# Kernel tuning notes

Hardware: AMD Instinct MI355X
Metric: run time of the kernel (lower is better)

## Reference

```python
import jax, jax.numpy as jnp
import numpy as np

POOL = 14
STRIDES = (4, 8, 16, 32)


def _roi_align(feat, boxes, bidx, scale, out=POOL):
    """Bilinear RoIAlign (1 sample per bin center). feat: [N,C,H,W], boxes: [M,4] image coords."""
    N, C, H, W = feat.shape
    b = boxes * scale
    x1, y1, x2, y2 = b[:, 0], b[:, 1], b[:, 2], b[:, 3]
    g = (jnp.arange(out, dtype=feat.dtype) + 0.5) / out
    xs = x1[:, None] + g[None, :] * (x2 - x1)[:, None]  # [M,out]
    ys = y1[:, None] + g[None, :] * (y2 - y1)[:, None]  # [M,out]
    x0f = jnp.floor(xs); y0f = jnp.floor(ys)
    lx = xs - x0f; ly = ys - y0f
    x0 = jnp.clip(x0f, 0, W - 1).astype(jnp.int32)
    x1i = jnp.clip(x0f + 1, 0, W - 1).astype(jnp.int32)
    y0 = jnp.clip(y0f, 0, H - 1).astype(jnp.int32)
    y1i = jnp.clip(y0f + 1, 0, H - 1).astype(jnp.int32)
    ft = jnp.transpose(feat, (0, 2, 3, 1))  # NHWC for trailing-channel gather
    bi = bidx[:, None, None]

    def gat(yy, xx):
        return ft[bi, yy[:, :, None], xx[:, None, :]]  # [M,out,out,C]

    wly = ly[:, :, None, None]; wlx = lx[:, None, :, None]
    val = (gat(y0, x0) * (1 - wly) * (1 - wlx)
           + gat(y0, x1i) * (1 - wly) * wlx
           + gat(y1i, x0) * wly * (1 - wlx)
           + gat(y1i, x1i) * wly * wlx)
    return jnp.transpose(val, (0, 3, 1, 2))  # [M,C,out,out]


def _fpn_levels(boxes, img_h, img_w):
    """Per-box FPN level: floor(4 + log2(sqrt(wh)/alpha)) mapped to pyramid index [0,3]."""
    alpha = 224.0 / 800.0 * float(min(img_h, img_w))
    bw = jnp.abs(boxes[:, 2] - boxes[:, 0])
    bh = jnp.abs(boxes[:, 3] - boxes[:, 1])
    s = jnp.sqrt(jnp.maximum(bw * bh, 1e-6))
    k = jnp.floor(4.0 + jnp.log2(s / alpha))
    return jnp.clip(k - 2.0, 0, 3).astype(jnp.int32)


def setup_inputs() -> dict:
    key = jax.random.key(0)
    ks = jax.random.split(key, 16)
    N, C, M, NCLS, HID = 2, 512, 512, 81, 1024
    p2 = jax.random.normal(ks[0], (N, C, 200, 200), jnp.float32)
    p3 = jax.random.normal(ks[1], (N, C, 100, 100), jnp.float32)
    p4 = jax.random.normal(ks[2], (N, C, 50, 50), jnp.float32)
    p5 = jax.random.normal(ks[3], (N, C, 25, 25), jnp.float32)
    cx = jax.random.uniform(ks[4], (M,), minval=100.0, maxval=700.0)
    cy = jax.random.uniform(ks[5], (M,), minval=100.0, maxval=700.0)
    bw = jax.random.uniform(ks[6], (M,), minval=32.0, maxval=400.0)
    bh = jax.random.uniform(ks[7], (M,), minval=32.0, maxval=400.0)
    boxes = jnp.stack([jnp.clip(cx - bw / 2, 0, 800), jnp.clip(cy - bh / 2, 0, 800),
                       jnp.clip(cx + bw / 2, 0, 800), jnp.clip(cy + bh / 2, 0, 800)], axis=1)
    batch_idx = jnp.repeat(jnp.arange(N, dtype=jnp.int32), M // N)
    w_fc1 = jax.random.normal(ks[8], (C * POOL * POOL, HID), jnp.float32) * 0.01
    b_fc1 = jnp.zeros((HID,), jnp.float32)
    w_cls = jax.random.normal(ks[9], (HID, NCLS), jnp.float32) * 0.05
    b_cls = jnp.zeros((NCLS,), jnp.float32)
    w_box = jax.random.normal(ks[10], (HID, NCLS), jnp.float32) * 0.05
    b_box = jnp.zeros((NCLS,), jnp.float32)
    w_conv = jax.random.normal(ks[11], (256, C, 3, 3), jnp.float32) * 0.02
    b_conv = jnp.zeros((256,), jnp.float32)
    w_mfc = jax.random.normal(ks[12], (256, NCLS), jnp.float32) * 0.05
    b_mfc = jnp.zeros((NCLS,), jnp.float32)
    return dict(p2=p2, p3=p3, p4=p4, p5=p5, boxes=boxes, batch_idx=batch_idx,
                w_fc1=w_fc1, b_fc1=b_fc1, w_cls=w_cls, b_cls=b_cls,
                w_box=w_box, b_box=b_box, w_conv=w_conv, b_conv=b_conv,
                w_mfc=w_mfc, b_mfc=b_mfc, img_h=800, img_w=800)


def reference(p2, p3, p4, p5, boxes, batch_idx, w_fc1, b_fc1, w_cls, b_cls,
              w_box, b_box, w_conv, b_conv, w_mfc, b_mfc, img_h, img_w):
    N = p2.shape[0]
    C = p2.shape[1]
    M = boxes.shape[0]
    num_classes = w_cls.shape[1]
    lvl = _fpn_levels(boxes, img_h, img_w)
    pooled = jnp.zeros((M, C, POOL, POOL), p2.dtype)
    for l, (feat, stride) in enumerate(zip([p2, p3, p4, p5], STRIDES)):
        pl = _roi_align(feat, boxes, batch_idx, 1.0 / stride)
        pooled = jnp.where((lvl == l)[:, None, None, None], pl, pooled)
    # cls / bbox head
    flat = pooled.reshape(M, -1)
    h = jax.nn.relu(flat @ w_fc1 + b_fc1)
    prob_cls = jax.nn.softmax(h @ w_cls + b_cls, axis=-1)
    reg_bbox = h @ w_box + b_box
    # mask head
    z = jax.lax.conv_general_dilated(pooled, w_conv, (1, 1), 'SAME',
                                     dimension_numbers=('NCHW', 'OIHW', 'NCHW'))
    z = jax.nn.relu(z + b_conv[None, :, None, None])
    prob_mask = jax.nn.sigmoid(jnp.mean(z, axis=(2, 3)) @ w_mfc + b_mfc)
    return (prob_cls.reshape(N, -1, num_classes),
            reg_bbox.reshape(N, -1, num_classes),
            prob_mask.reshape(N, -1, num_classes))
```

## Files before the change

kernel.cpp:

```cpp
#include <hip/hip_runtime.h>
#include <hip/hip_bf16.h>

#define POOLN 14
#define NBINS 196
#define CCH 512
#define MROIS 512
#define HIDD 1024
#define NCLS 81
#define KTOT 100352

typedef short short8 __attribute__((ext_vector_type(8)));
typedef __bf16 bf16x8 __attribute__((ext_vector_type(8)));
typedef float float4v __attribute__((ext_vector_type(4)));

__device__ __forceinline__ float4v mfma_bf16(bf16x8 a, bf16x8 b, float4v c) {
    return __builtin_amdgcn_mfma_f32_16x16x32_bf16(a, b, c, 0, 0, 0);
}

__device__ __forceinline__ unsigned short f2bf(float v) {
    __hip_bfloat16 h = __float2bfloat16(v);
    return __builtin_bit_cast(unsigned short, h);
}
__device__ __forceinline__ float bflo(unsigned int u) {
    return __builtin_bit_cast(float, u << 16);
}
__device__ __forceinline__ float bfhi(unsigned int u) {
    return __builtin_bit_cast(float, u & 0xFFFF0000u);
}

__device__ __forceinline__ void gload16(const void* g, void* l) {
    __builtin_amdgcn_global_load_lds(
        (const __attribute__((address_space(1))) unsigned int*)g,
        (__attribute__((address_space(3))) unsigned int*)l, 16, 0, 0);
}

__global__ void k_tr(const float* __restrict__ p2, const float* __restrict__ p3,
                     const float* __restrict__ p4, const float* __restrict__ p5,
                     unsigned short* __restrict__ f0, unsigned short* __restrict__ f1,
                     unsigned short* __restrict__ f2, unsigned short* __restrict__ f3) {
    __shared__ float tile[64 * 65];
    int pt = blockIdx.x;
    int n  = blockIdx.y >> 3;
    int c0 = (blockIdx.y & 7) * 64;
    const float* src; unsigned short* dst; int P;
    if (pt < 625)      { src = p2; dst = f0; P = 40000; }
    else if (pt < 782) { src = p3; dst = f1; P = 10000; pt -= 625; }
    else if (pt < 822) { src = p4; dst = f2; P = 2500;  pt -= 782; }
    else               { src = p5; dst = f3; P = 625;   pt -= 822; }
    int p0 = pt * 64;
    int t = threadIdx.x;
    #pragma unroll
    for (int i = 0; i < 16; ++i) {
        int idx = i * 256 + t;
        int pl = idx & 63, cl = idx >> 6;
        int p = p0 + pl;
        float v = 0.f;
        if (p < P) v = src[(size_t)(n * 512 + c0 + cl) * (size_t)P + p];
        tile[cl * 65 + pl] = v;
    }
    __syncthreads();
    #pragma unroll
    for (int i = 0; i < 8; ++i) {
        int idx = i * 256 + t;
        int cp = idx & 31, pl = idx >> 5;
        int p = p0 + pl;
        if (p < P) {
            unsigned int lo = (unsigned int)f2bf(tile[(cp * 2) * 65 + pl]);
            unsigned int hi = (unsigned int)f2bf(tile[(cp * 2 + 1) * 65 + pl]);
            *(unsigned int*)(dst + ((size_t)(n * (size_t)P + p) * 512 + c0 + cp * 2)) = lo | (hi << 16);
        }
    }
}

__global__ void k_roi(const unsigned short* __restrict__ f0, const unsigned short* __restrict__ f1,
                      const unsigned short* __restrict__ f2, const unsigned short* __restrict__ f3,
                      const float* __restrict__ boxes, const int* __restrict__ bidx,
                      const int* __restrict__ imh, const int* __restrict__ imw,
                      unsigned short* __restrict__ pooled) {
    int m = blockIdx.x;
    int t = threadIdx.x;
    float b0 = boxes[m*4+0], b1 = boxes[m*4+1], b2 = boxes[m*4+2], b3 = boxes[m*4+3];
    int ih = imh[0], iw = imw[0];
    float alpha = (224.0f/800.0f) * (float)(ih < iw ? ih : iw);
    float bw = fabsf(b2-b0), bh = fabsf(b3-b1);
    float s = sqrtf(fmaxf(bw*bh, 1e-6f));
    float kf = floorf(4.0f + log2f(s/alpha)) - 2.0f;
    int lvl = (int)fminf(fmaxf(kf, 0.0f), 3.0f);
    const unsigned short* f = lvl==0 ? f0 : (lvl==1 ? f1 : (lvl==2 ? f2 : f3));
    int W = 200 >> lvl;
    int P = W * W;
    float scale = 1.0f / (float)(4 << lvl);
    float x1s=b0*scale, y1s=b1*scale, x2s=b2*scale, y2s=b3*scale;
    const unsigned short* fb = f + (size_t)bidx[m] * (size_t)P * 512 + 2*t;
    unsigned short* outp = pooled + (size_t)m * NBINS * CCH + 2*t;
    float Wm1 = (float)(W-1);
    for (int py = 0; py < POOLN; ++py) {
        float gy = ((float)py + 0.5f) / 14.0f;
        float ys = y1s + gy * (y2s - y1s);
        float y0f = floorf(ys);
        float ly = ys - y0f;
        int y0 = (int)fminf(fmaxf(y0f, 0.0f), Wm1);
        int y1 = (int)fminf(fmaxf(y0f+1.0f, 0.0f), Wm1);
        #pragma unroll
        for (int px = 0; px < POOLN; ++px) {
            float gx = ((float)px + 0.5f) / 14.0f;
            float xs = x1s + gx * (x2s - x1s);
            float x0f = floorf(xs);
            float lx = xs - x0f;
            int x0 = (int)fminf(fmaxf(x0f, 0.0f), Wm1);
            int x1 = (int)fminf(fmaxf(x0f+1.0f, 0.0f), Wm1);
            unsigned int u00 = *(const unsigned int*)(fb + (size_t)(y0*W + x0) * 512);
            unsigned int u01 = *(const unsigned int*)(fb + (size_t)(y0*W + x1) * 512);
            unsigned int u10 = *(const unsigned int*)(fb + (size_t)(y1*W + x0) * 512);
            unsigned int u11 = *(const unsigned int*)(fb + (size_t)(y1*W + x1) * 512);
            float w00 = (1.0f-ly)*(1.0f-lx), w01 = (1.0f-ly)*lx;
            float w10 = ly*(1.0f-lx),        w11 = ly*lx;
            float vlo = bflo(u00)*w00 + bflo(u01)*w01 + bflo(u10)*w10 + bflo(u11)*w11;
            float vhi = bfhi(u00)*w00 + bfhi(u01)*w01 + bfhi(u10)*w10 + bfhi(u11)*w11;
            unsigned int r = (unsigned int)f2bf(vlo) | ((unsigned int)f2bf(vhi) << 16);
            *(unsigned int*)(outp + (size_t)(py*POOLN + px) * CCH) = r;
        }
    }
}

__global__ void k_pack_wfc1(const float* __restrict__ w, unsigned short* __restrict__ pk) {
    int g = blockIdx.x * 256 + threadIdx.x;
    int n = g & 1023;
    int k8 = g >> 10;
    int kp = k8 << 3;
    int p  = kp >> 9;
    int cc = kp & 511;
    short8 hv;
    #pragma unroll
    for (int j = 0; j < 8; ++j) {
        float v = w[(size_t)((cc+j)*NBINS + p) * HIDD + n];
        hv[j] = (short)f2bf(v);
    }
    *(short8*)(pk + (size_t)g * 8) = hv;
}

__global__ void k_pack_wconv(const float* __restrict__ w, unsigned short* __restrict__ wb) {
    int g = blockIdx.x * 256 + threadIdx.x;
    int c  = g & 511;
    int oc = (g >> 9) & 255;
    int kk = g >> 17;
    wb[g] = f2bf(w[(size_t)(oc*512 + c)*9 + kk]);
}

__launch_bounds__(256, 1)
__global__ void k_fc1(const unsigned short* __restrict__ A, const unsigned short* __restrict__ B,
                      float* __restrict__ part) {
    __shared__ unsigned short As[256*32];
    __shared__ unsigned short Bs[128*32];
    int t = threadIdx.x;
    int n0 = blockIdx.x * 128;
    int m0 = blockIdx.y * 256;
    int kz = blockIdx.z;
    int wave = t >> 6, ln = t & 63, ln15 = ln & 15, q = ln >> 4;
    int wr = (wave >> 1) * 128, wc = (wave & 1) * 64;
    int seg = ln & 3, rsub = ln >> 2;
    float4v acc[8][4];
    #pragma unroll
    for (int i = 0; i < 8; ++i)
        #pragma unroll
        for (int j = 0; j < 4; ++j) acc[i][j] = (float4v){0.f,0.f,0.f,0.f};
    int kbase = kz * 6272;
    for (int it = 0; it < 196; ++it) {
        int k0 = kbase + it*32;
        __syncthreads();
        #pragma unroll
        for (int i = 0; i < 4; ++i) {
            int row = i*64 + wave*16 + rsub;
            gload16(A + (size_t)(m0+row)*KTOT + k0 + seg*8, &As[(i*64 + wave*16)*32]);
        }
        #pragma unroll
        for (int i = 0; i < 2; ++i) {
            int nl = i*64 + wave*16 + rsub;
            gload16(B + ((size_t)((k0 >> 3) + seg)*1024 + n0 + nl)*8, &Bs[(i*64 + wave*16)*32]);
        }
        __syncthreads();
        bf16x8 bfr[4];
        #pragma unroll
        for (int ct = 0; ct < 4; ++ct)
            bfr[ct] = *(const bf16x8*)(&Bs[(wc + ct*16 + ln15)*32 + q*8]);
        #pragma unroll
        for (int rt = 0; rt < 8; ++rt) {
            bf16x8 af = *(const bf16x8*)(&As[(wr + rt*16 + ln15)*32 + q*8]);
            #pragma unroll
            for (int ct = 0; ct < 4; ++ct)
                acc[rt][ct] = mfma_bf16(af, bfr[ct], acc[rt][ct]);
        }
    }
    float* po = part + (size_t)kz * (MROIS*HIDD);
    #pragma unroll
    for (int rt = 0; rt < 8; ++rt)
        #pragma unroll
        for (int ct = 0; ct < 4; ++ct)
            #pragma unroll
            for (int r = 0; r < 4; ++r) {
                int row = m0 + wr + rt*16 + q*4 + r;
                int col = n0 + wc + ct*16 + ln15;
                po[(size_t)row*HIDD + col] = acc[rt][ct][r];
            }
}

__global__ void k_fc1_red(const float* __restrict__ part, const float* __restrict__ bias,
                          float* __restrict__ h) {
    int idx = blockIdx.x*256 + threadIdx.x;
    float s = 0.f;
    #pragma unroll
    for (int k = 0; k < 16; ++k) s += part[(size_t)k*524288 + idx];
    h[idx] = fmaxf(s + bias[idx & 1023], 0.f);
}

__launch_bounds__(512, 1)
__global__ void k_conv(const unsigned short* __restrict__ pooled, const unsigned short* __restrict__ wb,
                       const float* __restrict__ bconv, float* __restrict__ zmean) {
    __shared__ unsigned short As[208*32];
    __shared__ float sred[2][256];
    int m = blockIdx.x;
    int t = threadIdx.x;
    int wave = t >> 6, ln = t & 63, ln15 = ln & 15, q = ln >> 4;
    int og = wave & 3, mh = wave >> 2;
    int oc0 = og * 64;
    int rt0 = mh * 7;
    float4v acc[4][7];
    #pragma unroll
    for (int i = 0; i < 4; ++i)
        #pragma unroll
        for (int j = 0; j < 7; ++j) acc[i][j] = (float4v){0.f,0.f,0.f,0.f};
    const unsigned short* pm = pooled + (size_t)m * NBINS * CCH;
    const short8 Z8 = {0,0,0,0,0,0,0,0};
    int seg = ln & 3, rsub = ln >> 2;
    for (int ch = 0; ch < 16; ++ch) {
        int c0 = ch * 32;
        __syncthreads();
        #pragma unroll
        for (int i = 0; i < 2; ++i) {
            int wg = i*8 + wave;
            if (wg < 13) {
                int row = wg*16 + rsub;
                int rrow = row < 196 ? row : 195;
                gload16(pm + (size_t)rrow*CCH + c0 + seg*8, &As[(wg*16)*32]);
            }
        }
        __syncthreads();
        #pragma unroll
        for (int pos = 0; pos < 9; ++pos) {
            int dy = pos/3 - 1, dx = pos%3 - 1;
            bf16x8 bfr[4];
            #pragma unroll
            for (int oct = 0; oct < 4; ++oct)
                bfr[oct] = *(const bf16x8*)(wb + (size_t)(pos*256 + oc0 + oct*16 + ln15)*CCH + c0 + q*8);
            #pragma unroll
            for (int rr = 0; rr < 7; ++rr) {
                int rt = rt0 + rr;
                int p = rt*16 + ln15;
                int y = p / 14, x = p % 14;
                int yy = y + dy, xx = x + dx;
                bool valid = (p < 196) && ((unsigned)yy < 14u) && ((unsigned)xx < 14u);
                bf16x8 af = __builtin_bit_cast(bf16x8, Z8);
                if (valid) af = *(const bf16x8*)(&As[(yy*14+xx)*32 + q*8]);
                #pragma unroll
                for (int oct = 0; oct < 4; ++oct)
                    acc[oct][rr] = mfma_bf16(af, bfr[oct], acc[oct][rr]);
            }
        }
    }
    #pragma unroll
    for (int oct = 0; oct < 4; ++oct) {
        float b = bconv[oc0 + oct*16 + ln15];
        float s = 0.f;
        #pragma unroll
        for (int rr = 0; rr < 7; ++rr) {
            int rt = rt0 + rr;
            #pragma unroll
            for (int r = 0; r < 4; ++r) {
                int p = rt*16 + q*4 + r;
                if (p < 196) s += fmaxf(acc[oct][rr][r] + b, 0.f);
            }
        }
        s += __shfl_xor(s, 16, 64);
        s += __shfl_xor(s, 32, 64);
        if (ln < 16) sred[mh][oc0 + oct*16 + ln15] = s;
    }
    __syncthreads();
    if (t < 256) zmean[m*256 + t] = (sred[0][t] + sred[1][t]) * (1.0f/196.0f);
}

__global__ void k_cls(const float* __restrict__ h, const float* __restrict__ wcls,
                      const float* __restrict__ bcls, const float* __restrict__ wbox,
                      const float* __restrict__ bbox, float* __restrict__ out) {
    __shared__ float hs[HIDD];
    __shared__ float sc[NCLS];
    __shared__ float red[2];
    int m = blockIdx.x, t = threadIdx.x;
    #pragma unroll
    for (int i = 0; i < 8; ++i) hs[t + i*128] = h[(size_t)m*HIDD + t + i*128];
    __syncthreads();
    if (t < NCLS) {
        float ac = bcls[t], ab = bbox[t];
        #pragma unroll 4
        for (int k = 0; k < HIDD; ++k) {
            float hv = hs[k];
            ac += hv * wcls[k*NCLS + t];
            ab += hv * wbox[k*NCLS + t];
        }
        sc[t] = ac;
        out[41472 + m*NCLS + t] = ab;
    }
    __syncthreads();
    if (t == 0) {
        float mx = -3.0e38f;
        for (int i = 0; i < NCLS; ++i) mx = fmaxf(mx, sc[i]);
        red[0] = mx;
    }
    __syncthreads();
    if (t < NCLS) sc[t] = expf(sc[t] - red[0]);
    __syncthreads();
    if (t == 0) {
        float sm = 0.f;
        for (int i = 0; i < NCLS; ++i) sm += sc[i];
        red[1] = sm;
    }
    __syncthreads();
    if (t < NCLS) out[m*NCLS + t] = sc[t] / red[1];
}

__global__ void k_mask(const float* __restrict__ zmean, const float* __restrict__ wm,
                       const float* __restrict__ bm, float* __restrict__ out) {
    __shared__ float zs[256];
    int m = blockIdx.x, t = threadIdx.x;
    #pragma unroll
    for (int i = 0; i < 2; ++i) zs[t + i*128] = zmean[m*256 + t + i*128];
    __syncthreads();
    if (t < NCLS) {
        float a = bm[t];
        #pragma unroll 4
        for (int k = 0; k < 256; ++k) a += zs[k] * wm[k*NCLS + t];
        out[82944 + m*NCLS + t] = 1.0f / (1.0f + expf(-a));
    }
}

extern "C" void kernel_launch(void* const* d_in, const int* in_sizes, int n_in,
                              void* d_out, int out_size, void* d_ws, size_t ws_size,
                              hipStream_t stream) {
    (void)in_sizes; (void)n_in; (void)out_size; (void)ws_size;
    const float* p2    = (const float*)d_in[0];
    const float* p3    = (const float*)d_in[1];
    const float* p4    = (const float*)d_in[2];
    const float* p5    = (const float*)d_in[3];
    const float* boxes = (const float*)d_in[4];
    const int*   bidx  = (const int*)d_in[5];
    const float* wfc1  = (const float*)d_in[6];
    const float* bfc1  = (const float*)d_in[7];
    const float* wcls  = (const float*)d_in[8];
    const float* bcls  = (const float*)d_in[9];
    const float* wbox  = (const float*)d_in[10];
    const float* bbox  = (const float*)d_in[11];
    const float* wconv = (const float*)d_in[12];
    const float* bconv = (const float*)d_in[13];
    const float* wmfc  = (const float*)d_in[14];
    const float* bmfc  = (const float*)d_in[15];
    const int*   imh   = (const int*)d_in[16];
    const int*   imw   = (const int*)d_in[17];

    char* ws = (char*)d_ws;
    unsigned short* fpt0     = (unsigned short*)(ws);
    unsigned short* fpt1     = (unsigned short*)(ws + 81920000ull);
    unsigned short* fpt2     = (unsigned short*)(ws + 102400000ull);
    unsigned short* fpt3     = (unsigned short*)(ws + 107520000ull);
    unsigned short* packedB  = (unsigned short*)(ws);
    float*          partials = (float*)(ws + 205520896ull);
    float*          hbuf     = (float*)(ws + 239075328ull);
    float*          zmean    = (float*)(ws + 241172480ull);
    unsigned short* wconvb   = (unsigned short*)(ws + 241696768ull);
    unsigned short* pooled   = (unsigned short*)(ws + 244056064ull);
    float*          out      = (float*)d_out;

    hipLaunchKernelGGL(k_tr, dim3(832, 16), dim3(256), 0, stream,
                       p2, p3, p4, p5, fpt0, fpt1, fpt2, fpt3);
    hipLaunchKernelGGL(k_roi, dim3(512), dim3(256), 0, stream,
                       fpt0, fpt1, fpt2, fpt3, boxes, bidx, imh, imw, pooled);
    hipLaunchKernelGGL(k_pack_wfc1,  dim3(50176), dim3(256), 0, stream, wfc1, packedB);
    hipLaunchKernelGGL(k_pack_wconv, dim3(4608),  dim3(256), 0, stream, wconv, wconvb);
    hipLaunchKernelGGL(k_conv, dim3(512),  dim3(512), 0, stream, pooled, wconvb, bconv, zmean);
    hipLaunchKernelGGL(k_fc1,  dim3(8, 2, 16), dim3(256), 0, stream, pooled, packedB, partials);
    hipLaunchKernelGGL(k_fc1_red, dim3(2048), dim3(256), 0, stream, partials, bfc1, hbuf);
    hipLaunchKernelGGL(k_cls,  dim3(512), dim3(128), 0, stream, hbuf, wcls, bcls, wbox, bbox, out);
    hipLaunchKernelGGL(k_mask, dim3(512), dim3(128), 0, stream, zmean, wmfc, bmfc, out);
}
```

Baseline: 1.600 ms.

## Use MFMA for cls/box head and split conv by halves with padded LDS

```diff
diff --git a/kernel.cpp b/kernel.cpp
--- a/kernel.cpp
+++ b/kernel.cpp
@@ -139,12 +139,28 @@
     *(short8*)(pk + (size_t)g * 8) = hv;
 }
 
-__global__ void k_pack_wconv(const float* __restrict__ w, unsigned short* __restrict__ wb) {
+__global__ void k_pack_wconv(const float* __restrict__ w, unsigned short* __restrict__ wb,
+                             float* __restrict__ zmean) {
+    if (blockIdx.x >= 4608) {
+        int z = (blockIdx.x - 4608) * 256 + threadIdx.x;
+        zmean[z] = 0.f;
+        return;
+    }
     int g = blockIdx.x * 256 + threadIdx.x;
     int c  = g & 511;
     int oc = (g >> 9) & 255;
     int kk = g >> 17;
     wb[g] = f2bf(w[(size_t)(oc*512 + c)*9 + kk]);
+}
+
+__global__ void k_pack_whead(const float* __restrict__ wcls, const float* __restrict__ wbox,
+                             unsigned short* __restrict__ whb) {
+    int g = blockIdx.x * 256 + threadIdx.x;
+    int n = g >> 10, k = g & 1023;
+    float v = 0.f;
+    if (n < 81)       v = wcls[k*NCLS + n];
+    else if (n < 162) v = wbox[k*NCLS + (n-81)];
+    whb[g] = f2bf(v);
 }
 
 __launch_bounds__(256, 1)
@@ -205,62 +221,70 @@
 }
 
 __global__ void k_fc1_red(const float* __restrict__ part, const float* __restrict__ bias,
-                          float* __restrict__ h) {
+                          unsigned short* __restrict__ hb) {
     int idx = blockIdx.x*256 + threadIdx.x;
     float s = 0.f;
     #pragma unroll
     for (int k = 0; k < 16; ++k) s += part[(size_t)k*524288 + idx];
-    h[idx] = fmaxf(s + bias[idx & 1023], 0.f);
-}
-
-__launch_bounds__(512, 1)
+    hb[idx] = f2bf(fmaxf(s + bias[idx & 1023], 0.f));
+}
+
+__launch_bounds__(256, 2)
 __global__ void k_conv(const unsigned short* __restrict__ pooled, const unsigned short* __restrict__ wb,
                        const float* __restrict__ bconv, float* __restrict__ zmean) {
-    __shared__ unsigned short As[208*32];
-    __shared__ float sred[2][256];
-    int m = blockIdx.x;
+    __shared__ unsigned short As[161*40 + 8];
+    int mh = blockIdx.x;
+    int m  = blockIdx.y;
     int t = threadIdx.x;
     int wave = t >> 6, ln = t & 63, ln15 = ln & 15, q = ln >> 4;
-    int og = wave & 3, mh = wave >> 2;
-    int oc0 = og * 64;
-    int rt0 = mh * 7;
+    int oc0 = wave * 64;
+    {
+        unsigned int* a32 = (unsigned int*)As;
+        #pragma unroll
+        for (int i = 0; i < 13; ++i) {
+            int idx = i*256 + t;
+            if (idx < 3224) a32[idx] = 0u;
+        }
+    }
+    int soff[7];
+    #pragma unroll
+    for (int rr = 0; rr < 7; ++rr) {
+        int lp = rr*16 + ln15;
+        int yl = lp / 14, xl = lp - yl*14;
+        soff[rr] = ((yl + 1)*16 + xl + 1)*40 + q*8;
+    }
     float4v acc[4][7];
     #pragma unroll
     for (int i = 0; i < 4; ++i)
         #pragma unroll
         for (int j = 0; j < 7; ++j) acc[i][j] = (float4v){0.f,0.f,0.f,0.f};
-    const unsigned short* pm = pooled + (size_t)m * NBINS * CCH;
-    const short8 Z8 = {0,0,0,0,0,0,0,0};
-    int seg = ln & 3, rsub = ln >> 2;
+    const unsigned short* pm = pooled + (size_t)m * NBINS * CCH + (size_t)mh * 84 * CCH;
+    int sb0 = t >> 2, sseg0 = t & 3;
     for (int ch = 0; ch < 16; ++ch) {
         int c0 = ch * 32;
         __syncthreads();
         #pragma unroll
         for (int i = 0; i < 2; ++i) {
-            int wg = i*8 + wave;
-            if (wg < 13) {
-                int row = wg*16 + rsub;
-                int rrow = row < 196 ? row : 195;
-                gload16(pm + (size_t)rrow*CCH + c0 + seg*8, &As[(wg*16)*32]);
+            int g = i*256 + t;
+            if (g < 448) {
+                int b = g >> 2, seg = g & 3;
+                int yl = b / 14, xl = b - yl*14;
+                int r = yl + 1 - mh;
+                short8 v = *(const short8*)(pm + (size_t)b*CCH + c0 + seg*8);
+                *(short8*)(&As[(r*16 + xl + 1)*40 + seg*8]) = v;
             }
         }
         __syncthreads();
         #pragma unroll
         for (int pos = 0; pos < 9; ++pos) {
-            int dy = pos/3 - 1, dx = pos%3 - 1;
+            const int dy = pos/3 - 1, dx = pos%3 - 1;
             bf16x8 bfr[4];
             #pragma unroll
             for (int oct = 0; oct < 4; ++oct)
                 bfr[oct] = *(const bf16x8*)(wb + (size_t)(pos*256 + oc0 + oct*16 + ln15)*CCH + c0 + q*8);
             #pragma unroll
             for (int rr = 0; rr < 7; ++rr) {
-                int rt = rt0 + rr;
-                int p = rt*16 + ln15;
-                int y = p / 14, x = p % 14;
-                int yy = y + dy, xx = x + dx;
-                bool valid = (p < 196) && ((unsigned)yy < 14u) && ((unsigned)xx < 14u);
-                bf16x8 af = __builtin_bit_cast(bf16x8, Z8);
-                if (valid) af = *(const bf16x8*)(&As[(yy*14+xx)*32 + q*8]);
+                bf16x8 af = *(const bf16x8*)(&As[soff[rr] + (dy*16 + dx)*40]);
                 #pragma unroll
                 for (int oct = 0; oct < 4; ++oct)
                     acc[oct][rr] = mfma_bf16(af, bfr[oct], acc[oct][rr]);
@@ -272,59 +296,90 @@
         float b = bconv[oc0 + oct*16 + ln15];
         float s = 0.f;
         #pragma unroll
-        for (int rr = 0; rr < 7; ++rr) {
-            int rt = rt0 + rr;
+        for (int rr = 0; rr < 7; ++rr)
             #pragma unroll
             for (int r = 0; r < 4; ++r) {
-                int p = rt*16 + q*4 + r;
-                if (p < 196) s += fmaxf(acc[oct][rr][r] + b, 0.f);
-            }
-        }
+                int lp = rr*16 + q*4 + r;
+                if (lp < 98) s += fmaxf(acc[oct][rr][r] + b, 0.f);
+            }
         s += __shfl_xor(s, 16, 64);
         s += __shfl_xor(s, 32, 64);
-        if (ln < 16) sred[mh][oc0 + oct*16 + ln15] = s;
-    }
-    __syncthreads();
-    if (t < 256) zmean[m*256 + t] = (sred[0][t] + sred[1][t]) * (1.0f/196.0f);
-}
-
-__global__ void k_cls(const float* __restrict__ h, const float* __restrict__ wcls,
-                      const float* __restrict__ bcls, const float* __restrict__ wbox,
-                      const float* __restrict__ bbox, float* __restrict__ out) {
-    __shared__ float hs[HIDD];
-    __shared__ float sc[NCLS];
+        if (ln < 16) atomicAdd(&zmean[m*256 + oc0 + oct*16 + ln15], s * (1.0f/196.0f));
+    }
+}
+
+__launch_bounds__(256, 1)
+__global__ void k_head(const unsigned short* __restrict__ hb, const unsigned short* __restrict__ whb,
+                       const float* __restrict__ bcls, const float* __restrict__ bbox,
+                       float* __restrict__ sc, float* __restrict__ out) {
+    __shared__ unsigned short Ahs[128*40];
+    int t = threadIdx.x;
+    int m0 = blockIdx.x * 128;
+    int wave = t >> 6, ln = t & 63, ln15 = ln & 15, q = ln >> 4;
+    int wr = wave * 32;
+    float4v acc[2][11];
+    #pragma unroll
+    for (int i = 0; i < 2; ++i)
+        #pragma unroll
+        for (int j = 0; j < 11; ++j) acc[i][j] = (float4v){0.f,0.f,0.f,0.f};
+    for (int it = 0; it < 32; ++it) {
+        int k0 = it * 32;
+        __syncthreads();
+        #pragma unroll
+        for (int i = 0; i < 2; ++i) {
+            int g = i*256 + t;
+            int row = g >> 2, seg = g & 3;
+            short8 v = *(const short8*)(hb + (size_t)(m0+row)*HIDD + k0 + seg*8);
+            *(short8*)(&Ahs[row*40 + seg*8]) = v;
+        }
+        __syncthreads();
+        #pragma unroll
+        for (int ct = 0; ct < 11; ++ct) {
+            bf16x8 bfr = *(const bf16x8*)(whb + (size_t)(ct*16 + ln15)*HIDD + k0 + q*8);
+            #pragma unroll
+            for (int rt = 0; rt < 2; ++rt) {
+                bf16x8 af = *(const bf16x8*)(&Ahs[(wr + rt*16 + ln15)*40 + q*8]);
+                acc[rt][ct] = mfma_bf16(af, bfr, acc[rt][ct]);
+            }
+        }
+    }
+    #pragma unroll
+    for (int ct = 0; ct < 11; ++ct) {
+        int n = ct*16 + ln15;
+        float bc = (n < 81) ? bcls[n] : ((n < 162) ? bbox[n-81] : 0.f);
+        #pragma unroll
+        for (int rt = 0; rt < 2; ++rt)
+            #pragma unroll
+            for (int r = 0; r < 4; ++r) {
+                int row = m0 + wr + rt*16 + q*4 + r;
+                float v = acc[rt][ct][r] + bc;
+                if (n < 81)       sc[row*NCLS + n] = v;
+                else if (n < 162) out[41472 + row*NCLS + (n-81)] = v;
+            }
+    }
+}
+
+__global__ void k_softmax(const float* __restrict__ sc, float* __restrict__ out) {
+    __shared__ float v[NCLS];
     __shared__ float red[2];
     int m = blockIdx.x, t = threadIdx.x;
-    #pragma unroll
-    for (int i = 0; i < 8; ++i) hs[t + i*128] = h[(size_t)m*HIDD + t + i*128];
-    __syncthreads();
-    if (t < NCLS) {
-        float ac = bcls[t], ab = bbox[t];
-        #pragma unroll 4
-        for (int k = 0; k < HIDD; ++k) {
-            float hv = hs[k];
-            ac += hv * wcls[k*NCLS + t];
-            ab += hv * wbox[k*NCLS + t];
-        }
-        sc[t] = ac;
-        out[41472 + m*NCLS + t] = ab;
-    }
+    if (t < NCLS) v[t] = sc[m*NCLS + t];
     __syncthreads();
     if (t == 0) {
         float mx = -3.0e38f;
-        for (int i = 0; i < NCLS; ++i) mx = fmaxf(mx, sc[i]);
+        for (int i = 0; i < NCLS; ++i) mx = fmaxf(mx, v[i]);
         red[0] = mx;
     }
     __syncthreads();
-    if (t < NCLS) sc[t] = expf(sc[t] - red[0]);
+    if (t < NCLS) v[t] = expf(v[t] - red[0]);
     __syncthreads();
     if (t == 0) {
         float sm = 0.f;
-        for (int i = 0; i < NCLS; ++i) sm += sc[i];
+        for (int i = 0; i < NCLS; ++i) sm += v[i];
         red[1] = sm;
     }
     __syncthreads();
-    if (t < NCLS) out[m*NCLS + t] = sc[t] / red[1];
+    if (t < NCLS) out[m*NCLS + t] = v[t] / red[1];
 }
 
 __global__ void k_mask(const float* __restrict__ zmean, const float* __restrict__ wm,
@@ -372,9 +427,11 @@
     unsigned short* fpt3     = (unsigned short*)(ws + 107520000ull);
     unsigned short* packedB  = (unsigned short*)(ws);
     float*          partials = (float*)(ws + 205520896ull);
-    float*          hbuf     = (float*)(ws + 239075328ull);
-    float*          zmean    = (float*)(ws + 241172480ull);
-    unsigned short* wconvb   = (unsigned short*)(ws + 241696768ull);
+    unsigned short* hb       = (unsigned short*)(ws + 239075328ull);
+    float*          zmean    = (float*)(ws + 240123904ull);
+    unsigned short* wconvb   = (unsigned short*)(ws + 240648192ull);
+    unsigned short* whb      = (unsigned short*)(ws + 243007488ull);
+    float*          sc       = (float*)(ws + 243367936ull);
     unsigned short* pooled   = (unsigned short*)(ws + 244056064ull);
     float*          out      = (float*)d_out;
 
@@ -383,10 +440,12 @@
     hipLaunchKernelGGL(k_roi, dim3(512), dim3(256), 0, stream,
                        fpt0, fpt1, fpt2, fpt3, boxes, bidx, imh, imw, pooled);
     hipLaunchKernelGGL(k_pack_wfc1,  dim3(50176), dim3(256), 0, stream, wfc1, packedB);
-    hipLaunchKernelGGL(k_pack_wconv, dim3(4608),  dim3(256), 0, stream, wconv, wconvb);
-    hipLaunchKernelGGL(k_conv, dim3(512),  dim3(512), 0, stream, pooled, wconvb, bconv, zmean);
+    hipLaunchKernelGGL(k_pack_wconv, dim3(5120),  dim3(256), 0, stream, wconv, wconvb, zmean);
+    hipLaunchKernelGGL(k_pack_whead, dim3(704),   dim3(256), 0, stream, wcls, wbox, whb);
+    hipLaunchKernelGGL(k_conv, dim3(2, 512), dim3(256), 0, stream, pooled, wconvb, bconv, zmean);
     hipLaunchKernelGGL(k_fc1,  dim3(8, 2, 16), dim3(256), 0, stream, pooled, packedB, partials);
-    hipLaunchKernelGGL(k_fc1_red, dim3(2048), dim3(256), 0, stream, partials, bfc1, hbuf);
-    hipLaunchKernelGGL(k_cls,  dim3(512), dim3(128), 0, stream, hbuf, wcls, bcls, wbox, bbox, out);
+    hipLaunchKernelGGL(k_fc1_red, dim3(2048), dim3(256), 0, stream, partials, bfc1, hb);
+    hipLaunchKernelGGL(k_head, dim3(4), dim3(256), 0, stream, hb, whb, bcls, bbox, sc, out);
+    hipLaunchKernelGGL(k_softmax, dim3(512), dim3(128), 0, stream, sc, out);
     hipLaunchKernelGGL(k_mask, dim3(512), dim3(128), 0, stream, zmean, wmfc, bmfc, out);
 }
```

Result: faster. 1.547 ms (-3.3%).
